# Kernel tuning notes

Measured on AMD Instinct MI355X. Metric: run time of the kernel, lower is better.

## Reference

```python
import jax, jax.numpy as jnp
import numpy as np

B, S, D = 4, 4096, 256


def setup_inputs() -> dict:
    key = jax.random.key(0)
    k1, k2, k3, k4, k5 = jax.random.split(key, 5)
    query = jax.random.normal(k1, (B, S, D), dtype=jnp.float32)
    key_t = jax.random.normal(k2, (B, S, D), dtype=jnp.float32)
    value = jax.random.normal(k3, (B, S, D), dtype=jnp.float32)
    # nn.Linear(dim_model, dim_model): weight [D, D] (out, in), bias [D]
    bound = 1.0 / np.sqrt(D)
    Wq = jax.random.uniform(k4, (D, D), dtype=jnp.float32, minval=-bound, maxval=bound)
    bq = jax.random.uniform(k5, (D,), dtype=jnp.float32, minval=-bound, maxval=bound)
    return {"query": query, "key": key_t, "value": value, "Wq": Wq, "bq": bq}


def reference(query, key, value, Wq, bq):
    # Faithful to source: self.q is applied to ALL THREE inputs (source bug).
    q = jnp.einsum('bsd,od->bso', query, Wq) + bq  # [B,S,D]
    k = jnp.einsum('bsd,od->bso', key, Wq) + bq
    v = jnp.einsum('bsd,od->bso', value, Wq) + bq
    scale = jnp.sqrt(jnp.asarray(q.shape[-1], q.dtype))
    scores = jnp.einsum('bqd,bkd->bqk', q, k) / scale  # [B,S,S]
    attn = jax.nn.softmax(scores, axis=-1)
    return jnp.einsum('bqk,bkd->bqd', attn, v)  # [B,S,D]
```

## Files before the change

kernel.cpp:

```cpp
#include <hip/hip_runtime.h>


typedef __attribute__((ext_vector_type(4)))  float    f32x4;
typedef __attribute__((ext_vector_type(16))) float    f32x16;
typedef __attribute__((ext_vector_type(8)))  short    s16x8;
typedef __attribute__((ext_vector_type(2)))  unsigned u32x2;

#define AS_GLB const __attribute__((address_space(1))) unsigned
#define AS_LDS __attribute__((address_space(3))) unsigned

static constexpr float CEXP = 0.09016844f;
static constexpr float CM   = -32.0f * 0.09016844f;

static constexpr size_t QBF_OFF = 0;
static constexpr size_t KBF_OFF = 8ull  << 20;
static constexpr size_t VTB_OFF = 16ull << 20;
static constexpr size_t OT_OFF  = 24ull << 20;
static constexpr size_t LS_OFF  = 56ull << 20;

__device__ __forceinline__ unsigned bf16_rne(float f) {
  union { float f; unsigned u; } v; v.f = f;
  return (v.u + 0x7FFFu + ((v.u >> 16) & 1u)) >> 16;
}
__device__ __forceinline__ unsigned pkbf16(float a, float b) {
  return bf16_rne(a) | (bf16_rne(b) << 16);
}

__global__ __launch_bounds__(256, 2) void proj_kernel(
    const float* __restrict__ Xq, const float* __restrict__ Xk,
    const float* __restrict__ Xv, const float* __restrict__ Wq,
    const float* __restrict__ bq, char* __restrict__ ws)
{
  __shared__ char plds[32768];
  const int tid = threadIdx.x;
  const int lane = tid & 63, w = tid >> 6;
  const int wr = w >> 1, wc = w & 1;
  const int l15 = lane & 15, l4 = (lane >> 4) & 3;

  const int mt = blockIdx.x;
  const int tensor = mt >> 7;
  const int r0 = (mt & 127) << 7;
  const int n0 = blockIdx.y << 7;
  const float* A = (tensor == 0) ? Xq : (tensor == 1 ? Xk : Xv);

  f32x4 acc[4][4];
#pragma unroll
  for (int i = 0; i < 4; ++i)
#pragma unroll
    for (int j = 0; j < 4; ++j) { acc[i][j][0]=0.f; acc[i][j][1]=0.f; acc[i][j][2]=0.f; acc[i][j][3]=0.f; }

  for (int kt = 0; kt < 4; ++kt) {
    const int k0 = kt << 6;
#pragma unroll
    for (int j = 0; j < 8; ++j) {
      int c = j * 256 + tid;
      int row = c >> 4, col4 = c & 15;
      f32x4 av = *(const f32x4*)(A + (size_t)(r0 + row) * 256 + k0 + col4 * 4);
      u32x2 pa; pa[0] = pkbf16(av[0], av[1]); pa[1] = pkbf16(av[2], av[3]);
      int off = row * 128 + ((col4 * 8) ^ ((row & 7) << 4));
      *(u32x2*)(plds + off) = pa;
      f32x4 wv = *(const f32x4*)(Wq + (size_t)(n0 + row) * 256 + k0 + col4 * 4);
      u32x2 pw; pw[0] = pkbf16(wv[0], wv[1]); pw[1] = pkbf16(wv[2], wv[3]);
      *(u32x2*)(plds + 16384 + off) = pw;
    }
    __syncthreads();
#pragma unroll
    for (int ks = 0; ks < 2; ++ks) {
      s16x8 af[4], wf[4];
#pragma unroll
      for (int mi = 0; mi < 4; ++mi) {
        int row = wr * 64 + mi * 16 + l15;
        af[mi] = *(const s16x8*)(plds + row * 128 + ((ks * 64 + l4 * 16) ^ ((row & 7) << 4)));
      }
#pragma unroll
      for (int ni = 0; ni < 4; ++ni) {
        int row = wc * 64 + ni * 16 + l15;
        wf[ni] = *(const s16x8*)(plds + 16384 + row * 128 + ((ks * 64 + l4 * 16) ^ ((row & 7) << 4)));
      }
      if (tensor == 1) {
#pragma unroll
        for (int mi = 0; mi < 4; ++mi)
#pragma unroll
          for (int ni = 0; ni < 4; ++ni)
            acc[mi][ni] = __builtin_amdgcn_mfma_f32_16x16x32_bf16(wf[ni], af[mi], acc[mi][ni], 0, 0, 0);
      } else {
#pragma unroll
        for (int mi = 0; mi < 4; ++mi)
#pragma unroll
          for (int ni = 0; ni < 4; ++ni)
            acc[mi][ni] = __builtin_amdgcn_mfma_f32_16x16x32_bf16(af[mi], wf[ni], acc[mi][ni], 0, 0, 0);
      }
    }
    __syncthreads();
  }

  if (tensor == 0) {
    unsigned short* Qb = (unsigned short*)(ws + QBF_OFF);
#pragma unroll
    for (int ni = 0; ni < 4; ++ni) {
      int gn = n0 + wc * 64 + ni * 16 + l15;
      float bias = bq[gn];
#pragma unroll
      for (int mi = 0; mi < 4; ++mi) {
        int mrow = r0 + wr * 64 + mi * 16 + l4 * 4;
#pragma unroll
        for (int j = 0; j < 4; ++j)
          Qb[(size_t)(mrow + j) * 256 + gn] = (unsigned short)bf16_rne(acc[mi][ni][j] + bias);
      }
    }
  } else if (tensor == 1) {
    char* Kf = ws + KBF_OFF;
#pragma unroll
    for (int ni = 0; ni < 4; ++ni) {
      int dbase = n0 + wc * 64 + ni * 16 + l4 * 4;
      f32x4 bv = *(const f32x4*)(bq + dbase);
#pragma unroll
      for (int mi = 0; mi < 4; ++mi) {
        int s = r0 + wr * 64 + mi * 16 + l15;
        int b2 = s >> 12, sl = s & 31, kb = (s & 4095) >> 5;
        size_t chunk = (((size_t)b2 * 128 + kb) * 32 + (dbase >> 3)) * 32 + sl;
        u32x2 pv;
        pv[0] = pkbf16(acc[mi][ni][0] + bv[0], acc[mi][ni][1] + bv[1]);
        pv[1] = pkbf16(acc[mi][ni][2] + bv[2], acc[mi][ni][3] + bv[3]);
        *(u32x2*)(Kf + chunk * 16 + (dbase & 7) * 2) = pv;
      }
    }
  } else {
    char* Vf = ws + VTB_OFF;
#pragma unroll
    for (int ni = 0; ni < 4; ++ni) {
      int gn = n0 + wc * 64 + ni * 16 + l15;
      float bias = bq[gn];
#pragma unroll
      for (int mi = 0; mi < 4; ++mi) {
        int s = r0 + wr * 64 + mi * 16 + l4 * 4;
        int b2 = s >> 12, kb = (s & 4095) >> 5, sl = s & 31;
        size_t chunk = ((((size_t)b2 * 128 + kb) * 4 + (sl >> 3)) * 8 + (gn >> 5)) * 32 + (gn & 31);
        u32x2 pv;
        pv[0] = pkbf16(acc[mi][ni][0] + bias, acc[mi][ni][1] + bias);
        pv[1] = pkbf16(acc[mi][ni][2] + bias, acc[mi][ni][3] + bias);
        *(u32x2*)(Vf + chunk * 16 + (sl & 7) * 2) = pv;
      }
    }
  }
}

__global__ __launch_bounds__(256, 2) void flash_kernel(char* __restrict__ ws)
{
  __shared__ char lds[65536];
  const int tid = threadIdx.x;
  const int lane = tid & 63, w = tid >> 6;
  const int l31 = lane & 31, h = lane >> 5;

  const int bid  = blockIdx.x;
  const int sp   = bid & 3;
  const int b    = (bid >> 2) & 3;
  const int qblk = bid >> 4;
  const int q0w  = qblk * 128 + w * 32;
  const int kb0  = sp * 32;

  const char* Kfb = ws + KBF_OFF + (size_t)b * (2u << 20);
  const char* Vfb = ws + VTB_OFF + (size_t)b * (2u << 20);

  s16x8 qf[16];
  {
    const char* qrow = ws + QBF_OFF + (size_t)((b << 12) + q0w + l31) * 512 + h * 16;
#pragma unroll
    for (int i = 0; i < 16; ++i) qf[i] = *(const s16x8*)(qrow + i * 32);
  }
#pragma unroll
  for (int i = 0; i < 16; ++i) asm volatile("" :: "v"(qf[i]));

  f32x16 O[8];
#pragma unroll
  for (int t8 = 0; t8 < 8; ++t8)
#pragma unroll
    for (int r = 0; r < 16; ++r) O[t8][r] = 0.f;

  float l_run = 0.f;
  s16x8 paP0, paP1;

  auto STAGE_K = [&](int buf, int t) {
    const char* ksrc = Kfb + (size_t)(kb0 + t) * 16384;
#pragma unroll
    for (int i = 0; i < 4; ++i) {
      unsigned c = (unsigned)(w * 4 + i) << 10;
      __builtin_amdgcn_global_load_lds((AS_GLB*)(ksrc + c + (unsigned)lane * 16),
          (AS_LDS*)(lds + buf * 16384 + c), 16, 0, 0);
    }
  };
  auto STAGE_V = [&](int buf, int t) {
    const char* vsrc = Vfb + (size_t)(kb0 + t) * 16384;
#pragma unroll
    for (int i = 0; i < 4; ++i) {
      unsigned c = (unsigned)(w * 4 + i) << 10;
      __builtin_amdgcn_global_load_lds((AS_GLB*)(vsrc + c + (unsigned)lane * 16),
          (AS_LDS*)(lds + 32768 + buf * 16384 + c), 16, 0, 0);
    }
  };
  auto PV = [&](const char* vb, s16x8 a0, s16x8 a1) {
    __builtin_amdgcn_s_setprio(1);
#pragma unroll
    for (int t8 = 0; t8 < 8; ++t8) {
      s16x8 v0 = *(const s16x8*)(vb + ((h * 8 + t8) << 9) + l31 * 16);
      O[t8] = __builtin_amdgcn_mfma_f32_32x32x16_bf16(a0, v0, O[t8], 0, 0, 0);
      s16x8 v1 = *(const s16x8*)(vb + (((2 + h) * 8 + t8) << 9) + l31 * 16);
      O[t8] = __builtin_amdgcn_mfma_f32_32x32x16_bf16(a1, v1, O[t8], 0, 0, 0);
    }
    __builtin_amdgcn_s_setprio(0);
  };

  STAGE_K(0, 0);
  for (int t = 0; t < 32; ++t) {
    if (t + 1 < 32) STAGE_K((t + 1) & 1, t + 1);
    STAGE_V(t & 1, t);
    if (t + 1 < 32) { asm volatile("s_waitcnt vmcnt(8)" ::: "memory"); }
    else            { asm volatile("s_waitcnt vmcnt(4)" ::: "memory"); }
    __builtin_amdgcn_s_barrier();
    __builtin_amdgcn_sched_barrier(0);

    const char* kb = lds + (t & 1) * 16384;
    f32x16 pacc;
#pragma unroll
    for (int r = 0; r < 16; ++r) pacc[r] = 0.f;
    __builtin_amdgcn_s_setprio(1);
#pragma unroll
    for (int i = 0; i < 16; ++i) {
      s16x8 kf = *(const s16x8*)(kb + ((2 * i + h) << 9) + l31 * 16);
      pacc = __builtin_amdgcn_mfma_f32_32x32x16_bf16(kf, qf[i], pacc, 0, 0, 0);
    }
    __builtin_amdgcn_s_setprio(0);

    if (t > 0) PV(lds + 32768 + ((t - 1) & 1) * 16384, paP0, paP1);

    float p[16];
#pragma unroll
    for (int r = 0; r < 16; ++r)
      p[r] = __builtin_exp2f(__builtin_fmaf(pacc[r], CEXP, CM));
    float s0 = (p[0] + p[1]) + (p[2] + p[3]);
    float s1 = (p[4] + p[5]) + (p[6] + p[7]);
    float s2 = (p[8] + p[9]) + (p[10] + p[11]);
    float s3 = (p[12] + p[13]) + (p[14] + p[15]);
    l_run += (s0 + s1) + (s2 + s3);
    unsigned a0, a1, b0, b1, c0, c1, d0, d1;
    asm("v_cvt_pk_bf16_f32 %0, %1, %2" : "=v"(a0) : "v"(p[0]),  "v"(p[1]));
    asm("v_cvt_pk_bf16_f32 %0, %1, %2" : "=v"(a1) : "v"(p[2]),  "v"(p[3]));
    asm("v_cvt_pk_bf16_f32 %0, %1, %2" : "=v"(b0) : "v"(p[4]),  "v"(p[5]));
    asm("v_cvt_pk_bf16_f32 %0, %1, %2" : "=v"(b1) : "v"(p[6]),  "v"(p[7]));
    asm("v_cvt_pk_bf16_f32 %0, %1, %2" : "=v"(c0) : "v"(p[8]),  "v"(p[9]));
    asm("v_cvt_pk_bf16_f32 %0, %1, %2" : "=v"(c1) : "v"(p[10]), "v"(p[11]));
    asm("v_cvt_pk_bf16_f32 %0, %1, %2" : "=v"(d0) : "v"(p[12]), "v"(p[13]));
    asm("v_cvt_pk_bf16_f32 %0, %1, %2" : "=v"(d1) : "v"(p[14]), "v"(p[15]));
    asm("v_permlane32_swap_b32 %0, %1" : "+v"(a0), "+v"(b0));
    asm("v_permlane32_swap_b32 %0, %1" : "+v"(a1), "+v"(b1));
    asm("v_permlane32_swap_b32 %0, %1" : "+v"(c0), "+v"(d0));
    asm("v_permlane32_swap_b32 %0, %1" : "+v"(c1), "+v"(d1));
    union { s16x8 v; unsigned u[4]; } u0, u1;
    u0.u[0] = a0; u0.u[1] = a1; u0.u[2] = b0; u0.u[3] = b1;
    u1.u[0] = c0; u1.u[1] = c1; u1.u[2] = d0; u1.u[3] = d1;
    paP0 = u0.v; paP1 = u1.v;

    __builtin_amdgcn_s_barrier();
    __builtin_amdgcn_sched_barrier(0);
  }
  asm volatile("s_waitcnt vmcnt(0)" ::: "memory");
  __builtin_amdgcn_s_barrier();
  __builtin_amdgcn_sched_barrier(0);
  PV(lds + 32768 + 16384, paP0, paP1);

  l_run += __shfl_xor(l_run, 32, 64);

  unsigned short* OTb = (unsigned short*)(ws + OT_OFF) +
                        (((size_t)(sp * 4 + b) << 12) << 8);
#pragma unroll
  for (int t8 = 0; t8 < 8; ++t8) {
    int d = t8 * 32 + l31;
#pragma unroll
    for (int r = 0; r < 16; ++r) {
      int q = q0w + (r & 3) + 8 * (r >> 2) + 4 * h;
      OTb[(size_t)q * 256 + d] = (unsigned short)bf16_rne(O[t8][r]);
    }
  }
  if (lane < 32) {
    int idx = ((sp * 4 + b) << 12) + q0w + l31;
    ((float*)(ws + LS_OFF))[idx] = l_run;
  }
}

__global__ __launch_bounds__(256) void merge_kernel(const char* __restrict__ ws,
                                                    float* __restrict__ out)
{
  const int t = threadIdx.x;
  const int b = blockIdx.x;
  const int s0 = blockIdx.y << 4;
  const int soff = t >> 7, dd = (t & 127) * 2;
  const unsigned short* OTb = (const unsigned short*)(ws + OT_OFF);
  const float* Ls = (const float*)(ws + LS_OFF);
  for (int si = 0; si < 8; ++si) {
    int s = s0 + si * 2 + soff;
    float L = 0.f;
#pragma unroll
    for (int sp = 0; sp < 4; ++sp) L += Ls[((sp * 4 + b) << 12) + s];
    float rL = 1.0f / L;
    float a0 = 0.f, a1 = 0.f;
#pragma unroll
    for (int sp = 0; sp < 4; ++sp) {
      unsigned uv = *(const unsigned*)(OTb + ((((size_t)(sp * 4 + b) << 12) + s) << 8) + dd);
      union { unsigned u; float f; } lo, hi;
      lo.u = uv << 16; hi.u = uv & 0xFFFF0000u;
      a0 += lo.f; a1 += hi.f;
    }
    float2 o; o.x = a0 * rL; o.y = a1 * rL;
    *(float2*)(out + (((size_t)(b << 12) + s) << 8) + dd) = o;
  }
}

extern "C" void kernel_launch(void* const* d_in, const int* in_sizes, int n_in,
                              void* d_out, int out_size, void* d_ws, size_t ws_size,
                              hipStream_t stream) {
  const float* q  = (const float*)d_in[0];
  const float* k  = (const float*)d_in[1];
  const float* v  = (const float*)d_in[2];
  const float* Wq = (const float*)d_in[3];
  const float* bq = (const float*)d_in[4];
  char* ws = (char*)d_ws;
  float* out = (float*)d_out;
  hipLaunchKernelGGL(proj_kernel, dim3(384, 2), dim3(256), 0, stream, q, k, v, Wq, bq, ws);
  hipLaunchKernelGGL(flash_kernel, dim3(512), dim3(256), 0, stream, ws);
  hipLaunchKernelGGL(merge_kernel, dim3(4, 256), dim3(256), 0, stream, ws, out);
}
```

Before: 110.7 us.

## Interleave QK and PV MFMAs with split accumulators and restructure pipeline barriers

Each loop iteration now interleaves the QK^T MFMA chain for the current key tile with the PV MFMAs for the previous tile, so the matrix unit always has independent work queued. The score accumulator is split into even and odd halves to shorten the dependent MFMA chain, and the halves are summed before the exp. Synchronisation moves from a wait-then-barrier at the top to a single vmcnt(0)-plus-barrier at the end of each iteration, with the first and last iterations peeled out. The trade-off is that loads are now fully drained every iteration, giving less load lookahead, and the extra accumulator adds register pressure.

Measured after the change: 113.7 us. +2.8%, slower.

```diff
diff --git a/kernel.cpp b/kernel.cpp
--- a/kernel.cpp
+++ b/kernel.cpp
@@ -198,45 +198,12 @@
           (AS_LDS*)(lds + 32768 + buf * 16384 + c), 16, 0, 0);
     }
   };
-  auto PV = [&](const char* vb, s16x8 a0, s16x8 a1) {
-    __builtin_amdgcn_s_setprio(1);
-#pragma unroll
-    for (int t8 = 0; t8 < 8; ++t8) {
-      s16x8 v0 = *(const s16x8*)(vb + ((h * 8 + t8) << 9) + l31 * 16);
-      O[t8] = __builtin_amdgcn_mfma_f32_32x32x16_bf16(a0, v0, O[t8], 0, 0, 0);
-      s16x8 v1 = *(const s16x8*)(vb + (((2 + h) * 8 + t8) << 9) + l31 * 16);
-      O[t8] = __builtin_amdgcn_mfma_f32_32x32x16_bf16(a1, v1, O[t8], 0, 0, 0);
-    }
-    __builtin_amdgcn_s_setprio(0);
-  };
-
-  STAGE_K(0, 0);
-  for (int t = 0; t < 32; ++t) {
-    if (t + 1 < 32) STAGE_K((t + 1) & 1, t + 1);
-    STAGE_V(t & 1, t);
-    if (t + 1 < 32) { asm volatile("s_waitcnt vmcnt(8)" ::: "memory"); }
-    else            { asm volatile("s_waitcnt vmcnt(4)" ::: "memory"); }
-    __builtin_amdgcn_s_barrier();
-    __builtin_amdgcn_sched_barrier(0);
-
-    const char* kb = lds + (t & 1) * 16384;
-    f32x16 pacc;
-#pragma unroll
-    for (int r = 0; r < 16; ++r) pacc[r] = 0.f;
-    __builtin_amdgcn_s_setprio(1);
-#pragma unroll
-    for (int i = 0; i < 16; ++i) {
-      s16x8 kf = *(const s16x8*)(kb + ((2 * i + h) << 9) + l31 * 16);
-      pacc = __builtin_amdgcn_mfma_f32_32x32x16_bf16(kf, qf[i], pacc, 0, 0, 0);
-    }
-    __builtin_amdgcn_s_setprio(0);
-
-    if (t > 0) PV(lds + 32768 + ((t - 1) & 1) * 16384, paP0, paP1);
-
+
+  auto SOFTMAX_PACK = [&](const f32x16& pe, const f32x16& po) {
     float p[16];
 #pragma unroll
     for (int r = 0; r < 16; ++r)
-      p[r] = __builtin_exp2f(__builtin_fmaf(pacc[r], CEXP, CM));
+      p[r] = __builtin_exp2f(__builtin_fmaf(pe[r] + po[r], CEXP, CM));
     float s0 = (p[0] + p[1]) + (p[2] + p[3]);
     float s1 = (p[4] + p[5]) + (p[6] + p[7]);
     float s2 = (p[8] + p[9]) + (p[10] + p[11]);
@@ -259,14 +226,74 @@
     u0.u[0] = a0; u0.u[1] = a1; u0.u[2] = b0; u0.u[3] = b1;
     u1.u[0] = c0; u1.u[1] = c1; u1.u[2] = d0; u1.u[3] = d1;
     paP0 = u0.v; paP1 = u1.v;
-
-    __builtin_amdgcn_s_barrier();
-    __builtin_amdgcn_sched_barrier(0);
-  }
+  };
+
+  STAGE_K(0, 0);
   asm volatile("s_waitcnt vmcnt(0)" ::: "memory");
   __builtin_amdgcn_s_barrier();
   __builtin_amdgcn_sched_barrier(0);
-  PV(lds + 32768 + 16384, paP0, paP1);
+
+  {
+    STAGE_K(1, 1);
+    STAGE_V(0, 0);
+    const char* kb = lds;
+    f32x16 pe, po;
+#pragma unroll
+    for (int r = 0; r < 16; ++r) { pe[r] = 0.f; po[r] = 0.f; }
+    __builtin_amdgcn_s_setprio(1);
+#pragma unroll
+    for (int i = 0; i < 16; i += 2) {
+      s16x8 kf0 = *(const s16x8*)(kb + ((2 * i + h) << 9) + l31 * 16);
+      pe = __builtin_amdgcn_mfma_f32_32x32x16_bf16(kf0, qf[i], pe, 0, 0, 0);
+      s16x8 kf1 = *(const s16x8*)(kb + ((2 * (i + 1) + h) << 9) + l31 * 16);
+      po = __builtin_amdgcn_mfma_f32_32x32x16_bf16(kf1, qf[i + 1], po, 0, 0, 0);
+    }
+    __builtin_amdgcn_s_setprio(0);
+    SOFTMAX_PACK(pe, po);
+    asm volatile("s_waitcnt vmcnt(0)" ::: "memory");
+    __builtin_amdgcn_s_barrier();
+    __builtin_amdgcn_sched_barrier(0);
+  }
+
+  for (int t = 1; t < 32; ++t) {
+    if (t < 31) STAGE_K((t + 1) & 1, t + 1);
+    STAGE_V(t & 1, t);
+    const char* kb  = lds + (t & 1) * 16384;
+    const char* vbp = lds + 32768 + ((t + 1) & 1) * 16384;
+    f32x16 pe, po;
+#pragma unroll
+    for (int r = 0; r < 16; ++r) { pe[r] = 0.f; po[r] = 0.f; }
+    __builtin_amdgcn_s_setprio(1);
+#pragma unroll
+    for (int i = 0; i < 8; ++i) {
+      s16x8 kf0 = *(const s16x8*)(kb + ((4 * i + h) << 9) + l31 * 16);
+      pe = __builtin_amdgcn_mfma_f32_32x32x16_bf16(kf0, qf[2 * i], pe, 0, 0, 0);
+      s16x8 vv0 = *(const s16x8*)(vbp + ((h * 8 + i) << 9) + l31 * 16);
+      O[i] = __builtin_amdgcn_mfma_f32_32x32x16_bf16(paP0, vv0, O[i], 0, 0, 0);
+      s16x8 kf1 = *(const s16x8*)(kb + ((4 * i + 2 + h) << 9) + l31 * 16);
+      po = __builtin_amdgcn_mfma_f32_32x32x16_bf16(kf1, qf[2 * i + 1], po, 0, 0, 0);
+      s16x8 vv1 = *(const s16x8*)(vbp + (((2 + h) * 8 + i) << 9) + l31 * 16);
+      O[i] = __builtin_amdgcn_mfma_f32_32x32x16_bf16(paP1, vv1, O[i], 0, 0, 0);
+    }
+    __builtin_amdgcn_s_setprio(0);
+    SOFTMAX_PACK(pe, po);
+    asm volatile("s_waitcnt vmcnt(0)" ::: "memory");
+    __builtin_amdgcn_s_barrier();
+    __builtin_amdgcn_sched_barrier(0);
+  }
+
+  {
+    const char* vb = lds + 32768 + 16384;
+    __builtin_amdgcn_s_setprio(1);
+#pragma unroll
+    for (int t8 = 0; t8 < 8; ++t8) {
+      s16x8 v0 = *(const s16x8*)(vb + ((h * 8 + t8) << 9) + l31 * 16);
+      O[t8] = __builtin_amdgcn_mfma_f32_32x32x16_bf16(paP0, v0, O[t8], 0, 0, 0);
+      s16x8 v1 = *(const s16x8*)(vb + (((2 + h) * 8 + t8) << 9) + l31 * 16);
+      O[t8] = __builtin_amdgcn_mfma_f32_32x32x16_bf16(paP1, v1, O[t8], 0, 0, 0);
+    }
+    __builtin_amdgcn_s_setprio(0);
+  }
 
   l_run += __shfl_xor(l_run, 32, 64);
 
```
